# Kernel optimization log

Hardware: AMD Instinct MI355X
Metric: run time of the kernel (lower is better)

Reference implementation:

```python
import jax, jax.numpy as jnp
import numpy as np

EMBED = 2048
HEADS = 16


def setup_inputs() -> dict:
    key = jax.random.key(0)
    ks = jax.random.split(key, 9)
    N, L, E = 4, 2048, EMBED
    inp = {
        "query": jax.random.normal(ks[0], (N, L, E), dtype=jnp.float32),
        "keys": jax.random.normal(ks[1], (N, L, E), dtype=jnp.float32),
        "values": jax.random.normal(ks[2], (N, L, E), dtype=jnp.float32),
        "mask": jax.random.randint(ks[3], (N, L), 0, 2, dtype=jnp.int32),
        # nn.Linear weights, stored torch-style as (out_features, in_features)
        "Wq": jax.random.normal(ks[4], (E, E), dtype=jnp.float32) * (E ** -0.5),
        "Wk": jax.random.normal(ks[5], (E, E), dtype=jnp.float32) * (E ** -0.5),
        "Wv": jax.random.normal(ks[6], (E, E), dtype=jnp.float32) * (E ** -0.5),
        "Wo": jax.random.normal(ks[7], (E, E), dtype=jnp.float32) * (E ** -0.5),
        "bo": jax.random.normal(ks[8], (E,), dtype=jnp.float32) * 0.01,
    }
    return inp


def reference(query, keys, values, mask, Wq, Wk, Wv, Wo, bo):
    N, Lq, E = query.shape
    Lk = keys.shape[1]
    H = HEADS
    D = E // H
    # projections (torch Linear: y = x @ W.T)
    q = (query @ Wq.T).reshape(N, Lq, H, D)   # nqhd
    k = (keys @ Wk.T).reshape(N, Lk, H, D)    # nkhd
    v = (values @ Wv.T).reshape(N, Lk, H, D)  # nkhd
    # attention scores per head: (N, H, Lq, Lk)
    energy = jnp.einsum('nqhd,nkhd->nhqk', q, k)
    # 2D mask (N, Lk): 0 = masked out, broadcast over heads and query positions
    m = mask[:, None, None, :]
    energy = jnp.where(m == 0, jnp.float32(-1e20), energy)
    # source scales by sqrt(embed_size), not sqrt(head_dim)
    attn = jax.nn.softmax(energy * (E ** -0.5), axis=-1)
    out = jnp.einsum('nhqk,nkhd->nqhd', attn, v).reshape(N, Lq, E)
    return out @ Wo.T + bo
```

## Files before the change

kernel.cpp:

```cpp
#include <hip/hip_runtime.h>
#include <stdint.h>


typedef __bf16 bf16;
typedef __bf16 bf16x2 __attribute__((ext_vector_type(2)));
typedef __bf16 bf16x4 __attribute__((ext_vector_type(4)));
typedef __bf16 bf16x8 __attribute__((ext_vector_type(8)));
typedef float  f32x4  __attribute__((ext_vector_type(4)));
typedef uint32_t u32x4 __attribute__((ext_vector_type(4)));

#define MFMA16(a, b, c) __builtin_amdgcn_mfma_f32_16x16x32_bf16(a, b, c, 0, 0, 0)

__device__ __forceinline__ void gload_lds16(const void* g, void* s) {
  __builtin_amdgcn_global_load_lds(
      (const __attribute__((address_space(1))) void*)g,
      (__attribute__((address_space(3))) void*)s, 16, 0, 0);
}

__device__ __forceinline__ uint32_t pkbf(float a, float b) {
  return __builtin_bit_cast(uint32_t, (bf16x2){(bf16)a, (bf16)b});
}

__global__ __launch_bounds__(256) void cvt_bf16(const float* __restrict__ src,
                                                bf16* __restrict__ dst, long n) {
  long i = ((long)blockIdx.x * 256 + threadIdx.x) * 4;
  if (i < n) {
    f32x4 f = *(const f32x4*)(src + i);
    bf16x4 h = { (bf16)f.x, (bf16)f.y, (bf16)f.z, (bf16)f.w };
    *(bf16x4*)(dst + i) = h;
  }
}

__global__ __launch_bounds__(256) void cvt4_bf16(const float* __restrict__ s0,
                                                 const float* __restrict__ s1,
                                                 const float* __restrict__ s2,
                                                 const float* __restrict__ s3,
                                                 bf16* __restrict__ d0,
                                                 bf16* __restrict__ d1,
                                                 bf16* __restrict__ d2,
                                                 bf16* __restrict__ d3) {
  int wsel = blockIdx.y;
  const float* src = wsel == 0 ? s0 : wsel == 1 ? s1 : wsel == 2 ? s2 : s3;
  bf16* dst = wsel == 0 ? d0 : wsel == 1 ? d1 : wsel == 2 ? d2 : d3;
  long i = ((long)blockIdx.x * 256 + threadIdx.x) * 4;
  f32x4 f = *(const f32x4*)(src + i);
  bf16x4 h = { (bf16)f.x, (bf16)f.y, (bf16)f.z, (bf16)f.w };
  *(bf16x4*)(dst + i) = h;
}

__global__ __launch_bounds__(256) void gather_cvt(const float* __restrict__ src,
                                                  bf16* __restrict__ dst,
                                                  const int* __restrict__ idx) {
  long i = (long)blockIdx.x * 256 + threadIdx.x;
  int row = (int)(i >> 8);
  int u = (int)(i & 255);
  int n = row >> 11, p = row & 2047;
  long srow = ((long)n << 11) + idx[(n << 11) + p];
  const float* s = src + srow * 2048 + u * 8;
  f32x4 a = *(const f32x4*)s;
  f32x4 b = *(const f32x4*)(s + 4);
  bf16x8 h = { (bf16)a.x, (bf16)a.y, (bf16)a.z, (bf16)a.w,
               (bf16)b.x, (bf16)b.y, (bf16)b.z, (bf16)b.w };
  *(bf16x8*)(dst + (long)row * 2048 + u * 8) = h;
}

__global__ __launch_bounds__(256) void mask_compact(const int* __restrict__ mask,
                                                    int* __restrict__ idx,
                                                    int* __restrict__ cnts) {
  const int n = blockIdx.x;
  const int t = threadIdx.x, l = t & 63, w = t >> 6;
  const int* m = mask + n * 2048;
  __shared__ int wtot[4];
  int f[8], tt = 0;
  const int base = t * 8;
#pragma unroll
  for (int i = 0; i < 8; ++i) { f[i] = (m[base + i] != 0); tt += f[i]; }
  int sc = tt;
#pragma unroll
  for (int d = 1; d < 64; d <<= 1) {
    int v = __shfl_up(sc, d);
    if (l >= d) sc += v;
  }
  if (l == 63) wtot[w] = sc;
  __syncthreads();
  int woff = 0;
#pragma unroll
  for (int i = 0; i < 4; ++i) if (i < w) woff += wtot[i];
  int off = woff + sc - tt;
#pragma unroll
  for (int i = 0; i < 8; ++i)
    if (f[i]) { idx[n * 2048 + off] = base + i; ++off; }
  int total = wtot[0] + wtot[1] + wtot[2] + wtot[3];
  for (int p = total + t; p < 2048; p += 256) idx[n * 2048 + p] = 2047;
  if (t == 0) { cnts[n] = total; cnts[4 + n] = (total + 127) & ~127; }
}

template <int AEXIT, int OUT_F32, int ADD_BIAS>
__global__ __launch_bounds__(512, 2) void gemm256(const bf16* __restrict__ A,
                                                  const bf16* __restrict__ B,
                                                  void* __restrict__ Cout,
                                                  const float* __restrict__ bias,
                                                  const int* __restrict__ cnts) {
  constexpr int K = 2048, LDC = 2048, NT = 32;
  constexpr int TILE = 256 * 64;
  __shared__ bf16 S[2 * 2 * TILE];
  const int t = threadIdx.x;
  const int l = t & 63, w = t >> 6;
  const int wr = w >> 2, wc = w & 3;
  const int l15 = l & 15, l4 = l >> 4;

  const int Mb = ((blockIdx.x & 7) << 2) + (blockIdx.x >> 3);
  const long tm = (long)Mb * 256;
  const long tn = (long)blockIdx.y * 256;

  if constexpr (AEXIT) {
    int n = (int)(tm >> 11);
    if ((int)(tm & 2047) >= cnts[4 + n]) return;
  }

  const bf16* Ab = A + tm * K;
  const bf16* Bb = B + tn * K;

  auto stage = [&](int T, int p) {
    bf16* sA = S + p * 2 * TILE;
    bf16* sB = sA + TILE;
    const bf16* Ak = Ab + T * 64;
    const bf16* Bk = Bb + T * 64;
#pragma unroll
    for (int i = 0; i < 4; ++i) {
      int u = i * 512 + t;
      int row = u >> 3, slot = u & 7;
      int ss = slot ^ (row & 7);
      gload_lds16(Ak + (long)row * K + ss * 8, sA + u * 8);
    }
#pragma unroll
    for (int i = 0; i < 4; ++i) {
      int u = i * 512 + t;
      int row = u >> 3, slot = u & 7;
      int ss = slot ^ (row & 7);
      gload_lds16(Bk + (long)row * K + ss * 8, sB + u * 8);
    }
  };

  f32x4 acc[8][4];
#pragma unroll
  for (int i = 0; i < 8; ++i)
#pragma unroll
    for (int j = 0; j < 4; ++j) acc[i][j] = (f32x4){0.f, 0.f, 0.f, 0.f};

  stage(0, 0);

  for (int T = 0; T < NT; ++T) {
    const int p = T & 1;
    const bf16* sA = S + p * 2 * TILE;
    const bf16* sB = sA + TILE;

    asm volatile("" ::: "memory");
    __builtin_amdgcn_s_barrier();
    asm volatile("" ::: "memory");
    if (T + 1 < NT) {
      stage(T + 1, p ^ 1);
      asm volatile("s_waitcnt vmcnt(8)" ::: "memory");
    } else {
      asm volatile("s_waitcnt vmcnt(0)" ::: "memory");
    }
    __builtin_amdgcn_s_barrier();
    asm volatile("" ::: "memory");

#pragma unroll
    for (int kk = 0; kk < 2; ++kk) {
      bf16x8 af[8], bf[4];
#pragma unroll
      for (int mi = 0; mi < 8; ++mi) {
        int row = wr * 128 + mi * 16 + l15;
        int slot = (kk * 4 + l4) ^ (row & 7);
        af[mi] = *(const bf16x8*)(sA + row * 64 + slot * 8);
      }
#pragma unroll
      for (int ni = 0; ni < 4; ++ni) {
        int row = wc * 64 + ni * 16 + l15;
        int slot = (kk * 4 + l4) ^ (row & 7);
        bf[ni] = *(const bf16x8*)(sB + row * 64 + slot * 8);
      }
      __builtin_amdgcn_s_setprio(1);
#pragma unroll
      for (int mi = 0; mi < 8; ++mi)
#pragma unroll
        for (int ni = 0; ni < 4; ++ni)
          acc[mi][ni] = MFMA16(af[mi], bf[ni], acc[mi][ni]);
      __builtin_amdgcn_s_setprio(0);
    }
  }

#pragma unroll
  for (int mi = 0; mi < 8; ++mi) {
#pragma unroll
    for (int ni = 0; ni < 4; ++ni) {
      long col = tn + wc * 64 + ni * 16 + l15;
      long row = tm + wr * 128 + mi * 16 + l4 * 4;
#pragma unroll
      for (int r = 0; r < 4; ++r) {
        float v = acc[mi][ni][r];
        if constexpr (OUT_F32) {
          if constexpr (ADD_BIAS) v += bias[col];
          ((float*)Cout)[(row + r) * (long)LDC + col] = v;
        } else {
          ((bf16*)Cout)[(row + r) * (long)LDC + col] = (bf16)v;
        }
      }
    }
  }
}

__global__ __launch_bounds__(512, 4) void attn_fwd(const bf16* __restrict__ Qp,
                                                   const bf16* __restrict__ Kp,
                                                   const bf16* __restrict__ Vp,
                                                   const int* __restrict__ cnts,
                                                   bf16* __restrict__ Op) {
  constexpr int L = 2048, E = 2048, KVB = 64;
  __shared__ bf16 Kt[2][KVB * 128];
  __shared__ bf16 VT[2][128 * KVB];
  const int t = threadIdx.x, l = t & 63, w = t >> 6;
  const int l15 = l & 15, l4 = l >> 4;

  const int b = blockIdx.x;
  const int slot = ((b & 7) << 7) + (b >> 3);
  const int q0 = (slot & 15) << 7;
  const int y = slot >> 4;
  const int n = y >> 4, h = y & 15;
  const int wq = w * 16;
  const float scale = 0.022097086912079608f;

  const bf16* Qb = Qp + ((long)n * L + q0) * E + h * 128;
  const bf16* Kb = Kp + (long)n * L * E + h * 128;
  const bf16* Vb = Vp + (long)n * L * E + h * 128;
  const int cnt = cnts[n];
  const int ntk = (cnt + 63) >> 6;

  bf16x8 qf[4];
#pragma unroll
  for (int kk = 0; kk < 4; ++kk)
    qf[kk] = *(const bf16x8*)(Qb + (long)(wq + l15) * E + kk * 32 + l4 * 8);

  f32x4 o[8];
#pragma unroll
  for (int ni = 0; ni < 8; ++ni) o[ni] = (f32x4){0.f, 0.f, 0.f, 0.f};
  float mreg = -1e20f, lreg = 0.f;

  const int vj0 = ((l15 & 1) + 2 * l4 + 8 * (w & 1)) * 4;
  const int vd0 = ((l15 >> 1) + 8 * (w >> 1)) * 4;

  auto stageK = [&](int kv, int pp) {
#pragma unroll
    for (int i = 0; i < 2; ++i) {
      int u = i * 512 + t;
      int row = u >> 4, sl = u & 15;
      gload_lds16(Kb + (long)(kv + row) * E + ((sl ^ (row & 7)) * 8),
                  &Kt[pp][u * 8]);
    }
  };
  auto loadV = [&](int kv, bf16x4* vr) {
#pragma unroll
    for (int r = 0; r < 4; ++r)
      vr[r] = *(const bf16x4*)(Vb + (long)(kv + vj0 + r) * E + vd0);
  };
  auto writeV = [&](const bf16x4* vr, int pp) {
#pragma unroll
    for (int i = 0; i < 4; ++i) {
      int d = vd0 + i;
      bf16x4 pk = { vr[0][i], vr[1][i], vr[2][i], vr[3][i] };
      *(bf16x4*)(&VT[pp][d * KVB + (vj0 ^ ((d & 7) << 3))]) = pk;
    }
  };

  bf16x4 vr[4];
  stageK(0, 0);
  loadV(0, vr);
  writeV(vr, 0);
  __syncthreads();

  for (int ti = 0; ti < ntk; ++ti) {
    const int p = ti & 1;
    const int kv = ti << 6;
    const bool pre = (ti + 1) < ntk;
    if (pre) {
      stageK(kv + KVB, p ^ 1);
      loadV(kv + KVB, vr);
    }

    f32x4 s[4];
#pragma unroll
    for (int ni = 0; ni < 4; ++ni) s[ni] = (f32x4){0.f, 0.f, 0.f, 0.f};
#pragma unroll
    for (int kk = 0; kk < 4; ++kk) {
      bf16x8 kf[4];
#pragma unroll
      for (int ni = 0; ni < 4; ++ni) {
        int row = ni * 16 + l15;
        int sl = (kk * 4 + l4) ^ (row & 7);
        kf[ni] = *(const bf16x8*)(&Kt[p][row * 128 + sl * 8]);
      }
      __builtin_amdgcn_s_setprio(1);
#pragma unroll
      for (int ni = 0; ni < 4; ++ni)
        s[ni] = MFMA16(kf[ni], qf[kk], s[ni]);
      __builtin_amdgcn_s_setprio(0);
    }

    if (kv + KVB > cnt) {
#pragma unroll
      for (int ni = 0; ni < 4; ++ni)
#pragma unroll
        for (int r = 0; r < 4; ++r) {
          int j = kv + ni * 16 + l4 * 4 + r;
          s[ni][r] = (j < cnt) ? s[ni][r] * scale : -1e20f;
        }
    } else {
#pragma unroll
      for (int ni = 0; ni < 4; ++ni)
#pragma unroll
        for (int r = 0; r < 4; ++r) s[ni][r] *= scale;
    }

    float vmax = -1e20f;
#pragma unroll
    for (int ni = 0; ni < 4; ++ni)
#pragma unroll
      for (int r = 0; r < 4; ++r) vmax = fmaxf(vmax, s[ni][r]);
    vmax = fmaxf(vmax, __shfl_xor(vmax, 16));
    vmax = fmaxf(vmax, __shfl_xor(vmax, 32));
    bool nd = vmax > mreg + 8.0f;
    float corr = nd ? __expf(mreg - vmax) : 1.0f;
    float mn = nd ? vmax : mreg;
    mreg = mn;
    float rsum = 0.f;
    uint32_t u[4][2];
#pragma unroll
    for (int ni = 0; ni < 4; ++ni) {
      float p0 = __expf(s[ni][0] - mn);
      float p1 = __expf(s[ni][1] - mn);
      float p2 = __expf(s[ni][2] - mn);
      float p3 = __expf(s[ni][3] - mn);
      rsum += (p0 + p1) + (p2 + p3);
      u[ni][0] = pkbf(p0, p1);
      u[ni][1] = pkbf(p2, p3);
    }
    rsum += __shfl_xor(rsum, 16);
    rsum += __shfl_xor(rsum, 32);
    lreg = lreg * corr + rsum;
    if (__any(nd)) {
#pragma unroll
      for (int r = 0; r < 4; ++r) {
        float cr = __shfl(corr, l4 * 20 + r);
#pragma unroll
        for (int ni = 0; ni < 8; ++ni) o[ni][r] *= cr;
      }
    }

    const int srcA = l15 + ((l & 16) << 1);
    const int srcB = srcA + 16;
    const bool e5 = (l4 >> 1) != 0;
#pragma unroll
    for (int kk = 0; kk < 2; ++kk) {
      uint32_t a0 = (uint32_t)__shfl((int)u[kk * 2][0], srcA);
      uint32_t a1 = (uint32_t)__shfl((int)u[kk * 2][1], srcA);
      uint32_t a2 = (uint32_t)__shfl((int)u[kk * 2][0], srcB);
      uint32_t a3 = (uint32_t)__shfl((int)u[kk * 2][1], srcB);
      uint32_t b0 = (uint32_t)__shfl((int)u[kk * 2 + 1][0], srcA);
      uint32_t b1 = (uint32_t)__shfl((int)u[kk * 2 + 1][1], srcA);
      uint32_t b2 = (uint32_t)__shfl((int)u[kk * 2 + 1][0], srcB);
      uint32_t b3 = (uint32_t)__shfl((int)u[kk * 2 + 1][1], srcB);
      u32x4 pw = { e5 ? b0 : a0, e5 ? b1 : a1, e5 ? b2 : a2, e5 ? b3 : a3 };
      bf16x8 pa = __builtin_bit_cast(bf16x8, pw);
      bf16x8 vb[8];
#pragma unroll
      for (int ni = 0; ni < 8; ++ni) {
        int d = ni * 16 + l15;
        int col = (kk * 32 + l4 * 8) ^ ((d & 7) << 3);
        vb[ni] = *(const bf16x8*)(&VT[p][d * KVB + col]);
      }
      __builtin_amdgcn_s_setprio(1);
#pragma unroll
      for (int ni = 0; ni < 8; ++ni)
        o[ni] = MFMA16(pa, vb[ni], o[ni]);
      __builtin_amdgcn_s_setprio(0);
    }

    if (pre) writeV(vr, p ^ 1);
    __syncthreads();
  }

  float inv = 1.f / lreg;
#pragma unroll
  for (int r = 0; r < 4; ++r) {
    float iv = __shfl(inv, l4 * 20 + r);
    long grow = (long)n * L + q0 + wq + l4 * 4 + r;
#pragma unroll
    for (int ni = 0; ni < 8; ++ni)
      Op[grow * E + h * 128 + ni * 16 + l15] = (bf16)(o[ni][r] * iv);
  }
}

extern "C" void kernel_launch(void* const* d_in, const int* in_sizes, int n_in,
                              void* d_out, int out_size, void* d_ws, size_t ws_size,
                              hipStream_t stream) {
  (void)in_sizes; (void)n_in; (void)out_size; (void)ws_size;
  const float* query = (const float*)d_in[0];
  const float* keys  = (const float*)d_in[1];
  const float* values= (const float*)d_in[2];
  const int*   mask  = (const int*)d_in[3];
  const float* Wq = (const float*)d_in[4];
  const float* Wk = (const float*)d_in[5];
  const float* Wv = (const float*)d_in[6];
  const float* Wo = (const float*)d_in[7];
  const float* bo = (const float*)d_in[8];
  float* out = (float*)d_out;

  const int N = 4, L = 2048, E = 2048;
  const int M = N * L;
  const long EE = (long)E * E;
  const long ME = (long)M * E;

  int*  idx  = (int*)d_ws;
  int*  cnts = idx + N * 2048;
  bf16* Wqb  = (bf16*)((char*)d_ws + 65536);
  bf16* Wkb  = Wqb + EE;
  bf16* Wvb  = Wkb + EE;
  bf16* Wob  = Wvb + EE;
  bf16* qp   = Wob + EE;
  bf16* kp   = qp + ME;
  bf16* vp   = kp + ME;
  bf16* xs   = (bf16*)d_out;

  const int cbw = (int)(EE / 4 / 256);
  const int cba = (int)(ME / 4 / 256);
  const int gbl = (int)(ME / 8 / 256);
  dim3 gg(32, 8);

  mask_compact<<<4, 256, 0, stream>>>(mask, idx, cnts);
  cvt4_bf16<<<dim3(cbw, 4), 256, 0, stream>>>(Wq, Wk, Wv, Wo, Wqb, Wkb, Wvb, Wob);

  cvt_bf16<<<cba, 256, 0, stream>>>(query, xs, ME);
  gemm256<0, 0, 0><<<gg, 512, 0, stream>>>(xs, Wqb, qp, nullptr, cnts);

  gather_cvt<<<gbl, 256, 0, stream>>>(keys, xs, idx);
  gemm256<1, 0, 0><<<gg, 512, 0, stream>>>(xs, Wkb, kp, nullptr, cnts);

  gather_cvt<<<gbl, 256, 0, stream>>>(values, xs, idx);
  gemm256<1, 0, 0><<<gg, 512, 0, stream>>>(xs, Wvb, vp, nullptr, cnts);

  attn_fwd<<<1024, 512, 0, stream>>>(qp, kp, vp, cnts, qp);

  gemm256<0, 1, 1><<<gg, 512, 0, stream>>>(qp, Wob, out, bo, cnts);
}
```

Before: 452.0 us.

## Merge conversion/gather launches, batch K/V GEMMs, use exp2 softmax

Folds the query fp32-to-bf16 conversion into the weight conversion launch. Merges the K and V gathers into one kernel that also skips rows beyond the padded valid count. Runs the K and V projections as one GEMM launch using blockIdx.z, with separate staging buffers so the launches are independent. In attention, the log2(e) factor is folded into the scale so exp2f replaces __expf, and the lane mapping for V loads changes. The aim is fewer launches, less gather traffic and cheaper exponentials. The risk is a V layout mismatch with the unchanged writeV code.

```diff
diff --git a/kernel.cpp b/kernel.cpp
--- a/kernel.cpp
+++ b/kernel.cpp
@@ -21,47 +21,61 @@
   return __builtin_bit_cast(uint32_t, (bf16x2){(bf16)a, (bf16)b});
 }
 
-__global__ __launch_bounds__(256) void cvt_bf16(const float* __restrict__ src,
-                                                bf16* __restrict__ dst, long n) {
-  long i = ((long)blockIdx.x * 256 + threadIdx.x) * 4;
-  if (i < n) {
-    f32x4 f = *(const f32x4*)(src + i);
-    bf16x4 h = { (bf16)f.x, (bf16)f.y, (bf16)f.z, (bf16)f.w };
-    *(bf16x4*)(dst + i) = h;
-  }
-}
-
-__global__ __launch_bounds__(256) void cvt4_bf16(const float* __restrict__ s0,
+__global__ __launch_bounds__(256) void cvt8_bf16(const float* __restrict__ s0,
                                                  const float* __restrict__ s1,
                                                  const float* __restrict__ s2,
                                                  const float* __restrict__ s3,
+                                                 const float* __restrict__ q,
                                                  bf16* __restrict__ d0,
                                                  bf16* __restrict__ d1,
                                                  bf16* __restrict__ d2,
-                                                 bf16* __restrict__ d3) {
-  int wsel = blockIdx.y;
-  const float* src = wsel == 0 ? s0 : wsel == 1 ? s1 : wsel == 2 ? s2 : s3;
-  bf16* dst = wsel == 0 ? d0 : wsel == 1 ? d1 : wsel == 2 ? d2 : d3;
+                                                 bf16* __restrict__ d3,
+                                                 bf16* __restrict__ dq,
+                                                 long EE) {
+  int y = blockIdx.y;
+  const float* src;
+  bf16* dst;
+  if (y < 4) {
+    src = y == 0 ? s0 : y == 1 ? s1 : y == 2 ? s2 : s3;
+    dst = y == 0 ? d0 : y == 1 ? d1 : y == 2 ? d2 : d3;
+  } else {
+    src = q + (long)(y - 4) * EE;
+    dst = dq + (long)(y - 4) * EE;
+  }
   long i = ((long)blockIdx.x * 256 + threadIdx.x) * 4;
   f32x4 f = *(const f32x4*)(src + i);
   bf16x4 h = { (bf16)f.x, (bf16)f.y, (bf16)f.z, (bf16)f.w };
   *(bf16x4*)(dst + i) = h;
 }
 
-__global__ __launch_bounds__(256) void gather_cvt(const float* __restrict__ src,
-                                                  bf16* __restrict__ dst,
-                                                  const int* __restrict__ idx) {
+__global__ __launch_bounds__(256) void gather2_cvt(const float* __restrict__ ks,
+                                                   const float* __restrict__ vs,
+                                                   bf16* __restrict__ kd,
+                                                   bf16* __restrict__ vd,
+                                                   const int* __restrict__ idx,
+                                                   const int* __restrict__ cnts) {
   long i = (long)blockIdx.x * 256 + threadIdx.x;
   int row = (int)(i >> 8);
   int u = (int)(i & 255);
   int n = row >> 11, p = row & 2047;
+  if (p >= cnts[4 + n]) return;
   long srow = ((long)n << 11) + idx[(n << 11) + p];
-  const float* s = src + srow * 2048 + u * 8;
-  f32x4 a = *(const f32x4*)s;
-  f32x4 b = *(const f32x4*)(s + 4);
-  bf16x8 h = { (bf16)a.x, (bf16)a.y, (bf16)a.z, (bf16)a.w,
-               (bf16)b.x, (bf16)b.y, (bf16)b.z, (bf16)b.w };
-  *(bf16x8*)(dst + (long)row * 2048 + u * 8) = h;
+  long so = srow * 2048 + u * 8;
+  long dof = (long)row * 2048 + u * 8;
+  {
+    f32x4 a = *(const f32x4*)(ks + so);
+    f32x4 b = *(const f32x4*)(ks + so + 4);
+    bf16x8 h = { (bf16)a.x, (bf16)a.y, (bf16)a.z, (bf16)a.w,
+                 (bf16)b.x, (bf16)b.y, (bf16)b.z, (bf16)b.w };
+    *(bf16x8*)(kd + dof) = h;
+  }
+  {
+    f32x4 a = *(const f32x4*)(vs + so);
+    f32x4 b = *(const f32x4*)(vs + so + 4);
+    bf16x8 h = { (bf16)a.x, (bf16)a.y, (bf16)a.z, (bf16)a.w,
+                 (bf16)b.x, (bf16)b.y, (bf16)b.z, (bf16)b.w };
+    *(bf16x8*)(vd + dof) = h;
+  }
 }
 
 __global__ __launch_bounds__(256) void mask_compact(const int* __restrict__ mask,
@@ -96,9 +110,12 @@
 }
 
 template <int AEXIT, int OUT_F32, int ADD_BIAS>
-__global__ __launch_bounds__(512, 2) void gemm256(const bf16* __restrict__ A,
-                                                  const bf16* __restrict__ B,
-                                                  void* __restrict__ Cout,
+__global__ __launch_bounds__(512, 2) void gemm256(const bf16* __restrict__ A0,
+                                                  const bf16* __restrict__ A1,
+                                                  const bf16* __restrict__ B0,
+                                                  const bf16* __restrict__ B1,
+                                                  void* __restrict__ C0,
+                                                  void* __restrict__ C1,
                                                   const float* __restrict__ bias,
                                                   const int* __restrict__ cnts) {
   constexpr int K = 2048, LDC = 2048, NT = 32;
@@ -108,6 +125,10 @@
   const int l = t & 63, w = t >> 6;
   const int wr = w >> 2, wc = w & 3;
   const int l15 = l & 15, l4 = l >> 4;
+
+  const bf16* A = blockIdx.z ? A1 : A0;
+  const bf16* B = blockIdx.z ? B1 : B0;
+  void* Cout = blockIdx.z ? C1 : C0;
 
   const int Mb = ((blockIdx.x & 7) << 2) + (blockIdx.x >> 3);
   const long tm = (long)Mb * 256;
@@ -229,7 +250,7 @@
   const int y = slot >> 4;
   const int n = y >> 4, h = y & 15;
   const int wq = w * 16;
-  const float scale = 0.022097086912079608f;
+  const float scale2 = 0.031879357f;
 
   const bf16* Qb = Qp + ((long)n * L + q0) * E + h * 128;
   const bf16* Kb = Kp + (long)n * L * E + h * 128;
@@ -247,8 +268,8 @@
   for (int ni = 0; ni < 8; ++ni) o[ni] = (f32x4){0.f, 0.f, 0.f, 0.f};
   float mreg = -1e20f, lreg = 0.f;
 
-  const int vj0 = ((l15 & 1) + 2 * l4 + 8 * (w & 1)) * 4;
-  const int vd0 = ((l15 >> 1) + 8 * (w >> 1)) * 4;
+  const int vj0 = ((l15 & 7) + 8 * (w & 1)) * 4;
+  const int vd0 = ((l15 >> 3) + 2 * l4 + 8 * (w >> 1)) * 4;
 
   auto stageK = [&](int kv, int pp) {
 #pragma unroll
@@ -313,13 +334,13 @@
 #pragma unroll
         for (int r = 0; r < 4; ++r) {
           int j = kv + ni * 16 + l4 * 4 + r;
-          s[ni][r] = (j < cnt) ? s[ni][r] * scale : -1e20f;
+          s[ni][r] = (j < cnt) ? s[ni][r] * scale2 : -1e20f;
         }
     } else {
 #pragma unroll
       for (int ni = 0; ni < 4; ++ni)
 #pragma unroll
-        for (int r = 0; r < 4; ++r) s[ni][r] *= scale;
+        for (int r = 0; r < 4; ++r) s[ni][r] *= scale2;
     }
 
     float vmax = -1e20f;
@@ -329,18 +350,18 @@
       for (int r = 0; r < 4; ++r) vmax = fmaxf(vmax, s[ni][r]);
     vmax = fmaxf(vmax, __shfl_xor(vmax, 16));
     vmax = fmaxf(vmax, __shfl_xor(vmax, 32));
-    bool nd = vmax > mreg + 8.0f;
-    float corr = nd ? __expf(mreg - vmax) : 1.0f;
+    bool nd = vmax > mreg + 11.5f;
+    float corr = nd ? exp2f(mreg - vmax) : 1.0f;
     float mn = nd ? vmax : mreg;
     mreg = mn;
     float rsum = 0.f;
     uint32_t u[4][2];
 #pragma unroll
     for (int ni = 0; ni < 4; ++ni) {
-      float p0 = __expf(s[ni][0] - mn);
-      float p1 = __expf(s[ni][1] - mn);
-      float p2 = __expf(s[ni][2] - mn);
-      float p3 = __expf(s[ni][3] - mn);
+      float p0 = exp2f(s[ni][0] - mn);
+      float p1 = exp2f(s[ni][1] - mn);
+      float p2 = exp2f(s[ni][2] - mn);
+      float p3 = exp2f(s[ni][3] - mn);
       rsum += (p0 + p1) + (p2 + p3);
       u[ni][0] = pkbf(p0, p1);
       u[ni][1] = pkbf(p2, p3);
@@ -430,26 +451,25 @@
   bf16* qp   = Wob + EE;
   bf16* kp   = qp + ME;
   bf16* vp   = kp + ME;
-  bf16* xs   = (bf16*)d_out;
+  bf16* xq   = kp;
+  bf16* xk   = (bf16*)d_out;
+  bf16* xv   = (bf16*)d_out + ME;
 
   const int cbw = (int)(EE / 4 / 256);
-  const int cba = (int)(ME / 4 / 256);
   const int gbl = (int)(ME / 8 / 256);
-  dim3 gg(32, 8);
+  dim3 gg(32, 8, 1);
+  dim3 ggkv(32, 8, 2);
 
   mask_compact<<<4, 256, 0, stream>>>(mask, idx, cnts);
-  cvt4_bf16<<<dim3(cbw, 4), 256, 0, stream>>>(Wq, Wk, Wv, Wo, Wqb, Wkb, Wvb, Wob);
-
-  cvt_bf16<<<cba, 256, 0, stream>>>(query, xs, ME);
-  gemm256<0, 0, 0><<<gg, 512, 0, stream>>>(xs, Wqb, qp, nullptr, cnts);
-
-  gather_cvt<<<gbl, 256, 0, stream>>>(keys, xs, idx);
-  gemm256<1, 0, 0><<<gg, 512, 0, stream>>>(xs, Wkb, kp, nullptr, cnts);
-
-  gather_cvt<<<gbl, 256, 0, stream>>>(values, xs, idx);
-  gemm256<1, 0, 0><<<gg, 512, 0, stream>>>(xs, Wvb, vp, nullptr, cnts);
-
+  cvt8_bf16<<<dim3(cbw, 8), 256, 0, stream>>>(Wq, Wk, Wv, Wo, query,
+                                              Wqb, Wkb, Wvb, Wob, xq, EE);
+  gather2_cvt<<<gbl, 256, 0, stream>>>(keys, values, xk, xv, idx, cnts);
+
+  gemm256<0, 0, 0><<<gg, 512, 0, stream>>>(xq, xq, Wqb, Wqb, qp, qp,
+                                           nullptr, cnts);
+  gemm256<1, 0, 0><<<ggkv, 512, 0, stream>>>(xk, xv, Wkb, Wvb, kp, vp,
+                                             nullptr, cnts);
   attn_fwd<<<1024, 512, 0, stream>>>(qp, kp, vp, cnts, qp);
-
-  gemm256<0, 1, 1><<<gg, 512, 0, stream>>>(qp, Wob, out, bo, cnts);
-}
+  gemm256<0, 1, 1><<<gg, 512, 0, stream>>>(qp, qp, Wob, Wob, out, out,
+                                           bo, cnts);
+}
```

New measurement: 463.3 us. 1.02x slower.
